# Kernel optimization log

Measured on AMD Instinct MI355X. Metric: run time of the kernel, lower is better.

The kernel has to match this reference:

```python
import jax, jax.numpy as jnp
import numpy as np

EMB = 2048
N_HEADS = 32
N_KV_HEADS = 8
HEAD_DIM = EMB // N_HEADS
NUM_Q_PER_KV = N_HEADS // N_KV_HEADS


def setup_inputs() -> dict:
    key = jax.random.key(0)
    ks = jax.random.split(key, 7)
    B, S = 2, 2048
    scale = 1.0 / np.sqrt(EMB)
    return {
        "query": jax.random.normal(ks[0], (B, S, EMB), jnp.float32),
        "key": jax.random.normal(ks[1], (B, S, EMB), jnp.float32),
        "value": jax.random.normal(ks[2], (B, S, EMB), jnp.float32),
        "Wq": jax.random.normal(ks[3], (EMB, EMB), jnp.float32) * scale,
        "Wk": jax.random.normal(ks[4], (EMB, N_KV_HEADS * HEAD_DIM), jnp.float32) * scale,
        "Wv": jax.random.normal(ks[5], (EMB, N_KV_HEADS * HEAD_DIM), jnp.float32) * scale,
        "Wo": jax.random.normal(ks[6], (EMB, EMB), jnp.float32) * scale,
    }


def reference(query, key, value, Wq, Wk, Wv, Wo):
    B, Sq, _ = query.shape
    Skv = key.shape[1]
    # projections (Linear, no bias)
    q = (query @ Wq).reshape(B, Sq, N_HEADS, HEAD_DIM)            # [B,Sq,H,D]
    k = (key @ Wk).reshape(B, Skv, N_KV_HEADS, HEAD_DIM)          # [B,Skv,Hkv,D]
    v = (value @ Wv).reshape(B, Skv, N_KV_HEADS, HEAD_DIM)
    # repeat_kv: expand each kv head to num_q_per_kv query heads
    k = jnp.repeat(k, NUM_Q_PER_KV, axis=2)                       # [B,Skv,H,D]
    v = jnp.repeat(v, NUM_Q_PER_KV, axis=2)
    # attention
    scores = jnp.einsum('bqhd,bkhd->bhqk', q, k) / np.sqrt(HEAD_DIM)
    probs = jax.nn.softmax(scores, axis=-1)                       # [B,H,Sq,Skv]
    ctx = jnp.einsum('bhqk,bkhd->bqhd', probs, v)                 # [B,Sq,H,D]
    ctx = ctx.reshape(B, Sq, EMB)
    return ctx @ Wo
```

## Files before the change

kernel.cpp:

```cpp
#include <hip/hip_runtime.h>
#include <hip/hip_bf16.h>
#include <stdint.h>

#define EMB   2048
#define HQ    32
#define NKV   8
#define HD    64
#define BATCH 2
#define SEQ   2048
#define MR    (BATCH * SEQ)
#define KVD   (NKV * HD)

using bfrag = __attribute__((ext_vector_type(8))) short;
using facc  = __attribute__((ext_vector_type(4))) float;

__device__ __forceinline__ unsigned short f32_bf16(float f) {
  union { float f; uint32_t u; } v;
  v.f = f;
  return (unsigned short)((v.u + 0x7fffu + ((v.u >> 16) & 1u)) >> 16);
}
__device__ __forceinline__ uint32_t pk2(float a, float b) {
  __hip_bfloat162 h = __float22bfloat162_rn(make_float2(a, b));
  uint32_t u; __builtin_memcpy(&u, &h, 4); return u;
}
__device__ __forceinline__ float fexp2(float x) {
#if __has_builtin(__builtin_amdgcn_exp2f)
  return __builtin_amdgcn_exp2f(x);
#else
  return exp2f(x);
#endif
}

__device__ __forceinline__ void gl2lds16(const void* g, void* l) {
  __builtin_amdgcn_global_load_lds((__attribute__((address_space(1))) void*)g,
                                   (__attribute__((address_space(3))) void*)l,
                                   16, 0, 0);
}

__device__ __forceinline__ void swz_mn_n(int bid, int nwg, int& m0, int& n0) {
  const int sw = (bid & 7) * (nwg >> 3) + (bid >> 3);
  m0 = (sw & 31) << 7;
  n0 = (sw >> 5) << 7;
}

__global__ __launch_bounds__(256) void kprep(const float* __restrict__ q_in,
                                             unsigned short* __restrict__ qbf,
                                             const float* __restrict__ Wq,
                                             const float* __restrict__ Wk,
                                             const float* __restrict__ Wv,
                                             const float* __restrict__ Wo,
                                             unsigned short* __restrict__ WqT,
                                             unsigned short* __restrict__ WkT,
                                             unsigned short* __restrict__ WvT,
                                             unsigned short* __restrict__ WoT,
                                             float qscale) {
  __shared__ unsigned short t[32][33];
  int bid = blockIdx.x;
  if (bid < 4096) {
    const size_t i0 = ((size_t)bid * 256 + threadIdx.x) * 8;
    const float4 f0 = *(const float4*)(q_in + i0);
    const float4 f1 = *(const float4*)(q_in + i0 + 4);
    uint4 w;
    w.x = pk2(f0.x * qscale, f0.y * qscale);
    w.y = pk2(f0.z * qscale, f0.w * qscale);
    w.z = pk2(f1.x * qscale, f1.y * qscale);
    w.w = pk2(f1.z * qscale, f1.w * qscale);
    *(uint4*)(qbf + i0) = w;
    return;
  }
  bid -= 4096;
  const float* in; unsigned short* out; int C;
  if (bid < 4096)      { in = Wq; out = WqT; C = 2048; }
  else if (bid < 5120) { bid -= 4096; in = Wk; out = WkT; C = 512; }
  else if (bid < 6144) { bid -= 5120; in = Wv; out = WvT; C = 512; }
  else                 { bid -= 6144; in = Wo; out = WoT; C = 2048; }
  const int R = 2048, CB = C >> 5;
  const int c0 = (bid % CB) * 32, r0 = (bid / CB) * 32;
  const int tx = threadIdx.x & 31, ty = threadIdx.x >> 5;
#pragma unroll
  for (int i = 0; i < 32; i += 8)
    t[ty + i][tx] = f32_bf16(in[(size_t)(r0 + ty + i) * C + (c0 + tx)]);
  __syncthreads();
#pragma unroll
  for (int i = 0; i < 32; i += 8)
    out[(size_t)(c0 + ty + i) * R + (r0 + tx)] = t[tx][ty + i];
}

__global__ __launch_bounds__(256) void kproj(const unsigned short* __restrict__ qbf,
                                             const float* __restrict__ k_in,
                                             const float* __restrict__ v_in,
                                             const unsigned short* __restrict__ WqT,
                                             const unsigned short* __restrict__ WkT,
                                             const unsigned short* __restrict__ WvT,
                                             unsigned short* __restrict__ qp,
                                             unsigned short* __restrict__ kp,
                                             unsigned short* __restrict__ vT) {
  __shared__ __align__(16) unsigned short As[128][32];
  __shared__ __align__(16) unsigned short Bs[128][32];
  int bid = blockIdx.x;
  int mode, N, lnwg;
  const unsigned short* Bt;
  if (bid < 512)      { mode = 0; Bt = WqT; N = 2048; lnwg = 512; }
  else if (bid < 640) { mode = 1; Bt = WkT; N = 512; lnwg = 128; bid -= 512; }
  else                { mode = 2; Bt = WvT; N = 512; lnwg = 128; bid -= 640; }
  int m0, n0; swz_mn_n(bid, lnwg, m0, n0);

  const int tid  = threadIdx.x;
  const int wv   = tid >> 6;
  const int lane = tid & 63;
  const int quad = lane >> 4;
  const int l15  = lane & 15;
  const int wm = (wv >> 1) * 64;
  const int wn = (wv & 1) * 64;
  const int K = EMB;

  const facc fzero = {0.f, 0.f, 0.f, 0.f};
  facc acc[4][4];
#pragma unroll
  for (int i = 0; i < 4; ++i)
#pragma unroll
    for (int j = 0; j < 4; ++j) acc[i][j] = fzero;

  const float* ain = (mode == 1) ? k_in : v_in;
  const int e0 = wv * 1024 + lane * 8;
  for (int k0 = 0; k0 < K; k0 += 32) {
    if (mode == 0) {
#pragma unroll
      for (int u = 0; u < 2; ++u) {
        const int e = e0 + u * 512;
        const int r = e >> 5, c = e & 31;
        gl2lds16(qbf + (size_t)(m0 + r) * K + (k0 + c), (unsigned short*)As + e);
        gl2lds16(Bt  + (size_t)(n0 + r) * K + (k0 + c), (unsigned short*)Bs + e);
      }
    } else {
#pragma unroll
      for (int u = 0; u < 2; ++u) {
        const int e = e0 + u * 512;
        const int r = e >> 5, c = e & 31;
        gl2lds16(Bt + (size_t)(n0 + r) * K + (k0 + c), (unsigned short*)Bs + e);
        const float* ap = ain + (size_t)(m0 + r) * K + (k0 + c);
        const float4 f0 = *(const float4*)ap;
        const float4 f1 = *(const float4*)(ap + 4);
        uint4 w;
        w.x = pk2(f0.x, f0.y);
        w.y = pk2(f0.z, f0.w);
        w.z = pk2(f1.x, f1.y);
        w.w = pk2(f1.z, f1.w);
        *(uint4*)((unsigned short*)As + e) = w;
      }
    }
    __syncthreads();
    bfrag af[4], bf[4];
#pragma unroll
    for (int i = 0; i < 4; ++i) af[i] = *(const bfrag*)&As[wm + i * 16 + l15][quad * 8];
#pragma unroll
    for (int j = 0; j < 4; ++j) bf[j] = *(const bfrag*)&Bs[wn + j * 16 + l15][quad * 8];
#pragma unroll
    for (int i = 0; i < 4; ++i)
#pragma unroll
      for (int j = 0; j < 4; ++j)
        acc[i][j] = __builtin_amdgcn_mfma_f32_16x16x32_bf16(af[i], bf[j], acc[i][j], 0, 0, 0);
    __syncthreads();
  }

  if (mode < 2) {
    unsigned short* Cp = (mode == 0) ? qp : kp;
#pragma unroll
    for (int i = 0; i < 4; ++i)
#pragma unroll
      for (int j = 0; j < 4; ++j) {
        const int col = n0 + wn + j * 16 + l15;
        const size_t base = (size_t)(m0 + wm + i * 16 + quad * 4) * N + col;
#pragma unroll
        for (int r = 0; r < 4; ++r)
          Cp[base + (size_t)r * N] = f32_bf16(acc[i][j][r]);
      }
  } else {
#pragma unroll
    for (int i = 0; i < 4; ++i)
#pragma unroll
      for (int j = 0; j < 4; ++j) {
        const int n = n0 + wn + j * 16 + l15;
        const int m = m0 + wm + i * 16 + quad * 4;
        uint2 w;
        w.x = pk2(acc[i][j][0], acc[i][j][1]);
        w.y = pk2(acc[i][j][2], acc[i][j][3]);
        *(uint2*)(vT + (size_t)n * MR + m) = w;
      }
  }
}

__global__ __launch_bounds__(256) void kgemm_bt_f32out(const unsigned short* __restrict__ A,
                                                       const unsigned short* __restrict__ Bt,
                                                       float* __restrict__ C,
                                                       int M, int N, int K) {
  __shared__ __align__(16) unsigned short As[128][32];
  __shared__ __align__(16) unsigned short Bs[128][32];
  const int tid  = threadIdx.x;
  const int wv   = tid >> 6;
  const int lane = tid & 63;
  const int quad = lane >> 4;
  const int l15  = lane & 15;
  int m0, n0; swz_mn_n(blockIdx.x, gridDim.x, m0, n0);
  const int wm = (wv >> 1) * 64;
  const int wn = (wv & 1) * 64;

  const facc fzero = {0.f, 0.f, 0.f, 0.f};
  facc acc[4][4];
#pragma unroll
  for (int i = 0; i < 4; ++i)
#pragma unroll
    for (int j = 0; j < 4; ++j) acc[i][j] = fzero;

  const int e0 = wv * 1024 + lane * 8;
  for (int k0 = 0; k0 < K; k0 += 32) {
#pragma unroll
    for (int u = 0; u < 2; ++u) {
      const int e = e0 + u * 512;
      const int r = e >> 5, c = e & 31;
      gl2lds16(A  + (size_t)(m0 + r) * K + (k0 + c), (unsigned short*)As + e);
      gl2lds16(Bt + (size_t)(n0 + r) * K + (k0 + c), (unsigned short*)Bs + e);
    }
    __syncthreads();
    bfrag af[4], bf[4];
#pragma unroll
    for (int i = 0; i < 4; ++i) af[i] = *(const bfrag*)&As[wm + i * 16 + l15][quad * 8];
#pragma unroll
    for (int j = 0; j < 4; ++j) bf[j] = *(const bfrag*)&Bs[wn + j * 16 + l15][quad * 8];
#pragma unroll
    for (int i = 0; i < 4; ++i)
#pragma unroll
      for (int j = 0; j < 4; ++j)
        acc[i][j] = __builtin_amdgcn_mfma_f32_16x16x32_bf16(af[i], bf[j], acc[i][j], 0, 0, 0);
    __syncthreads();
  }

#pragma unroll
  for (int i = 0; i < 4; ++i)
#pragma unroll
    for (int j = 0; j < 4; ++j) {
      const int col = n0 + wn + j * 16 + l15;
      const size_t base = (size_t)(m0 + wm + i * 16 + quad * 4) * N + col;
#pragma unroll
      for (int r = 0; r < 4; ++r)
        C[base + (size_t)r * N] = acc[i][j][r];
    }
}

__device__ __forceinline__ unsigned short* psa(unsigned short* p, int row, int colShort) {
  return (unsigned short*)((char*)p + ((row << 7) + (((colShort << 1)) ^ ((row & 7) << 4))));
}
__device__ __forceinline__ const bfrag* tfrag(const unsigned short* base, int r, int c) {
  return (const bfrag*)(base + (size_t)r * 64 + ((c ^ (r & 7)) << 3));
}

__global__ __launch_bounds__(128, 2) void kattn(const unsigned short* __restrict__ Qp,
                                                const unsigned short* __restrict__ Kp,
                                                const unsigned short* __restrict__ Vt,
                                                unsigned short* __restrict__ Ctx) {
  __shared__ __align__(16) unsigned short Ps[2][64][64];
  __shared__ __align__(16) unsigned short Kb[2][64 * 64];
  __shared__ __align__(16) unsigned short Vs[64 * 64];

  const int tid  = threadIdx.x;
  const int wv   = tid >> 6;
  const int lane = tid & 63;
  const int quad = lane >> 4;
  const int l15  = lane & 15;
  const int q0  = blockIdx.x * 128;
  const int h   = blockIdx.y;
  const int b   = blockIdx.z;
  const int kvh = h >> 2;

  unsigned short* ps = &Ps[wv][0][0];

  const unsigned short* qbase = Qp + (size_t)(b * SEQ + q0 + wv * 64) * EMB + h * HD;
  bfrag qf[2][4];
#pragma unroll
  for (int kk = 0; kk < 2; ++kk)
#pragma unroll
    for (int j = 0; j < 4; ++j)
      qf[kk][j] = *(const bfrag*)(qbase + (size_t)(j * 16 + l15) * EMB + kk * 32 + quad * 8);

  const facc fzero = {0.f, 0.f, 0.f, 0.f};
  float l_st[4];
  facc o[4][4];
#pragma unroll
  for (int j = 0; j < 4; ++j) l_st[j] = 0.f;
#pragma unroll
  for (int i = 0; i < 4; ++i)
#pragma unroll
    for (int j = 0; j < 4; ++j) o[i][j] = fzero;

  const unsigned short* kg = Kp + (size_t)(b * SEQ) * KVD + kvh * HD;
  const unsigned short* vg = Vt + (size_t)(kvh * HD) * MR + b * SEQ;
  const int r8  = lane >> 3;
  const int sc8 = ((lane & 7) ^ r8) * 8;

#pragma unroll
  for (int u = 0; u < 4; ++u) {
    const int row = (wv * 4 + u) * 8 + r8;
    gl2lds16(kg + (size_t)row * KVD + sc8, &Kb[0][(wv * 4 + u) * 512]);
  }

  for (int kt = 0; kt < SEQ / 64; ++kt) {
    const int cur = kt & 1;
    __asm__ __volatile__("s_waitcnt vmcnt(0)" ::: "memory");
    __builtin_amdgcn_s_barrier();
    __asm__ __volatile__("" ::: "memory");

#pragma unroll
    for (int u = 0; u < 4; ++u) {
      const int row = (wv * 4 + u) * 8 + r8;
      gl2lds16(vg + (size_t)row * MR + kt * 64 + sc8, &Vs[(wv * 4 + u) * 512]);
    }
    const int ktn = (kt < SEQ / 64 - 1) ? kt + 1 : kt;
#pragma unroll
    for (int u = 0; u < 4; ++u) {
      const int row = (wv * 4 + u) * 8 + r8;
      gl2lds16(kg + (size_t)(ktn * 64 + row) * KVD + sc8, &Kb[cur ^ 1][(wv * 4 + u) * 512]);
    }

    const unsigned short* kb = &Kb[cur][0];
    float rs[4] = {0.f, 0.f, 0.f, 0.f};
#pragma unroll
    for (int i = 0; i < 4; ++i) {
      const bfrag af0 = *tfrag(kb, i * 16 + l15, quad);
      const bfrag af1 = *tfrag(kb, i * 16 + l15, 4 + quad);
      facc s[4];
#pragma unroll
      for (int j = 0; j < 4; ++j) s[j] = fzero;
      __builtin_amdgcn_s_setprio(1);
#pragma unroll
      for (int j = 0; j < 4; ++j)
        s[j] = __builtin_amdgcn_mfma_f32_16x16x32_bf16(af0, qf[0][j], s[j], 0, 0, 0);
#pragma unroll
      for (int j = 0; j < 4; ++j)
        s[j] = __builtin_amdgcn_mfma_f32_16x16x32_bf16(af1, qf[1][j], s[j], 0, 0, 0);
      __builtin_amdgcn_s_setprio(0);
#pragma unroll
      for (int j = 0; j < 4; ++j) {
        const float p0 = fexp2(s[j][0]);
        const float p1 = fexp2(s[j][1]);
        const float p2 = fexp2(s[j][2]);
        const float p3 = fexp2(s[j][3]);
        rs[j] += (p0 + p1) + (p2 + p3);
        uint2 w;
        w.x = pk2(p0, p1);
        w.y = pk2(p2, p3);
        *(uint2*)psa(ps, j * 16 + l15, i * 16 + quad * 4) = w;
      }
    }

#pragma unroll
    for (int j = 0; j < 4; ++j) {
      float r = rs[j];
      r += __shfl_xor(r, 16, 64);
      r += __shfl_xor(r, 32, 64);
      l_st[j] += r;
    }

    __asm__ __volatile__("s_waitcnt vmcnt(4)" ::: "memory");
    __builtin_amdgcn_s_barrier();
    __asm__ __volatile__("" ::: "memory");

    __builtin_amdgcn_s_setprio(1);
#pragma unroll
    for (int kk = 0; kk < 2; ++kk) {
      bfrag bpf[4], vf[4];
#pragma unroll
      for (int j = 0; j < 4; ++j)
        bpf[j] = *(const bfrag*)psa(ps, j * 16 + l15, kk * 32 + quad * 8);
#pragma unroll
      for (int id = 0; id < 4; ++id)
        vf[id] = *tfrag(Vs, id * 16 + l15, kk * 4 + quad);
#pragma unroll
      for (int id = 0; id < 4; ++id)
#pragma unroll
        for (int j = 0; j < 4; ++j)
          o[id][j] = __builtin_amdgcn_mfma_f32_16x16x32_bf16(vf[id], bpf[j], o[id][j], 0, 0, 0);
    }
    __builtin_amdgcn_s_setprio(0);
  }

#pragma unroll
  for (int j = 0; j < 4; ++j) {
    const float inv = 1.f / l_st[j];
#pragma unroll
    for (int id = 0; id < 4; ++id) {
      uint2 w;
      w.x = pk2(o[id][j][0] * inv, o[id][j][1] * inv);
      w.y = pk2(o[id][j][2] * inv, o[id][j][3] * inv);
      *(uint2*)psa(ps, j * 16 + l15, id * 16 + quad * 4) = w;
    }
  }
  __asm__ __volatile__("" ::: "memory");
#pragma unroll
  for (int s = 0; s < 8; ++s) {
    const int r  = (lane >> 2) + 16 * (s & 3);
    const int cb = (lane & 3) * 8 + 32 * (s >> 2);
    const uint4 t = *(const uint4*)psa(ps, r, cb);
    const size_t row = (size_t)(b * SEQ + q0 + wv * 64 + r);
    *(uint4*)&Ctx[row * EMB + h * HD + cb] = t;
  }
}

extern "C" void kernel_launch(void* const* d_in, const int* in_sizes, int n_in,
                              void* d_out, int out_size, void* d_ws, size_t ws_size,
                              hipStream_t stream) {
  (void)in_sizes; (void)n_in; (void)out_size; (void)ws_size;
  const float* q_in = (const float*)d_in[0];
  const float* k_in = (const float*)d_in[1];
  const float* v_in = (const float*)d_in[2];
  const float* Wq   = (const float*)d_in[3];
  const float* Wk   = (const float*)d_in[4];
  const float* Wv   = (const float*)d_in[5];
  const float* Wo   = (const float*)d_in[6];
  float* out = (float*)d_out;

  char* ws = (char*)d_ws;
  unsigned short* WqT = (unsigned short*)(ws);
  unsigned short* WkT = (unsigned short*)(ws + (size_t)( 8u << 20));
  unsigned short* WvT = (unsigned short*)(ws + (size_t)(10u << 20));
  unsigned short* WoT = (unsigned short*)(ws + (size_t)(12u << 20));
  unsigned short* qbf = (unsigned short*)(ws + (size_t)(20u << 20));
  unsigned short* qp  = (unsigned short*)(ws + (size_t)(36u << 20));
  unsigned short* kp  = (unsigned short*)(ws + (size_t)(52u << 20));
  unsigned short* vT  = (unsigned short*)(ws + (size_t)(56u << 20));
  unsigned short* ctx = qbf;

  kprep<<<14336, 256, 0, stream>>>(q_in, qbf, Wq, Wk, Wv, Wo,
                                   WqT, WkT, WvT, WoT, 0.18033688011112042f);
  kproj<<<768, 256, 0, stream>>>(qbf, k_in, v_in, WqT, WkT, WvT, qp, kp, vT);
  kattn<<<dim3(16, 32, 2), 128, 0, stream>>>(qp, kp, vT, ctx);
  kgemm_bt_f32out<<<512, 256, 0, stream>>>(ctx, WoT, out, MR, EMB, EMB);
}
```

Measured before the change: 396.5 us.

## Double-buffer LDS tiles in Q projection and output GEMM loops

Adds a second LDS buffer for the A and B tiles in the Q-projection path of kproj and in the output-projection GEMM. The next K-slice is prefetched with direct global-to-LDS loads while MFMAs consume the current slice, and one barrier per iteration is removed. The goal is to hide global load latency behind compute. LDS use per block doubles, which may reduce occupancy. Correctness depends on the async gl2lds load completing before the single barrier at the end of each iteration.

```diff
diff --git a/kernel.cpp b/kernel.cpp
--- a/kernel.cpp
+++ b/kernel.cpp
@@ -95,8 +95,8 @@
                                              unsigned short* __restrict__ qp,
                                              unsigned short* __restrict__ kp,
                                              unsigned short* __restrict__ vT) {
-  __shared__ __align__(16) unsigned short As[128][32];
-  __shared__ __align__(16) unsigned short Bs[128][32];
+  __shared__ __align__(16) unsigned short As[2][4096];
+  __shared__ __align__(16) unsigned short Bs[2][4096];
   int bid = blockIdx.x;
   int mode, N, lnwg;
   const unsigned short* Bt;
@@ -121,23 +121,53 @@
 #pragma unroll
     for (int j = 0; j < 4; ++j) acc[i][j] = fzero;
 
-  const float* ain = (mode == 1) ? k_in : v_in;
   const int e0 = wv * 1024 + lane * 8;
-  for (int k0 = 0; k0 < K; k0 += 32) {
-    if (mode == 0) {
+
+  if (mode == 0) {
+#pragma unroll
+    for (int u = 0; u < 2; ++u) {
+      const int e = e0 + u * 512;
+      const int r = e >> 5, c = e & 31;
+      gl2lds16(qbf + (size_t)(m0 + r) * K + c, &As[0][e]);
+      gl2lds16(Bt  + (size_t)(n0 + r) * K + c, &Bs[0][e]);
+    }
+    __syncthreads();
+    int cur = 0;
+    const int NT = K >> 5;
+    for (int t = 0; t < NT; ++t) {
+      if (t + 1 < NT) {
+        const int k1 = (t + 1) << 5;
+#pragma unroll
+        for (int u = 0; u < 2; ++u) {
+          const int e = e0 + u * 512;
+          const int r = e >> 5, c = e & 31;
+          gl2lds16(qbf + (size_t)(m0 + r) * K + k1 + c, &As[cur ^ 1][e]);
+          gl2lds16(Bt  + (size_t)(n0 + r) * K + k1 + c, &Bs[cur ^ 1][e]);
+        }
+      }
+      bfrag af[4], bf[4];
+#pragma unroll
+      for (int i = 0; i < 4; ++i)
+        af[i] = *(const bfrag*)&As[cur][(wm + i * 16 + l15) * 32 + quad * 8];
+#pragma unroll
+      for (int j = 0; j < 4; ++j)
+        bf[j] = *(const bfrag*)&Bs[cur][(wn + j * 16 + l15) * 32 + quad * 8];
+#pragma unroll
+      for (int i = 0; i < 4; ++i)
+#pragma unroll
+        for (int j = 0; j < 4; ++j)
+          acc[i][j] = __builtin_amdgcn_mfma_f32_16x16x32_bf16(af[i], bf[j], acc[i][j], 0, 0, 0);
+      __syncthreads();
+      cur ^= 1;
+    }
+  } else {
+    const float* ain = (mode == 1) ? k_in : v_in;
+    for (int k0 = 0; k0 < K; k0 += 32) {
 #pragma unroll
       for (int u = 0; u < 2; ++u) {
         const int e = e0 + u * 512;
         const int r = e >> 5, c = e & 31;
-        gl2lds16(qbf + (size_t)(m0 + r) * K + (k0 + c), (unsigned short*)As + e);
-        gl2lds16(Bt  + (size_t)(n0 + r) * K + (k0 + c), (unsigned short*)Bs + e);
-      }
-    } else {
-#pragma unroll
-      for (int u = 0; u < 2; ++u) {
-        const int e = e0 + u * 512;
-        const int r = e >> 5, c = e & 31;
-        gl2lds16(Bt + (size_t)(n0 + r) * K + (k0 + c), (unsigned short*)Bs + e);
+        gl2lds16(Bt + (size_t)(n0 + r) * K + (k0 + c), &Bs[0][e]);
         const float* ap = ain + (size_t)(m0 + r) * K + (k0 + c);
         const float4 f0 = *(const float4*)ap;
         const float4 f1 = *(const float4*)(ap + 4);
@@ -146,21 +176,23 @@
         w.y = pk2(f0.z, f0.w);
         w.z = pk2(f1.x, f1.y);
         w.w = pk2(f1.z, f1.w);
-        *(uint4*)((unsigned short*)As + e) = w;
-      }
-    }
-    __syncthreads();
-    bfrag af[4], bf[4];
-#pragma unroll
-    for (int i = 0; i < 4; ++i) af[i] = *(const bfrag*)&As[wm + i * 16 + l15][quad * 8];
-#pragma unroll
-    for (int j = 0; j < 4; ++j) bf[j] = *(const bfrag*)&Bs[wn + j * 16 + l15][quad * 8];
-#pragma unroll
-    for (int i = 0; i < 4; ++i)
-#pragma unroll
-      for (int j = 0; j < 4; ++j)
-        acc[i][j] = __builtin_amdgcn_mfma_f32_16x16x32_bf16(af[i], bf[j], acc[i][j], 0, 0, 0);
-    __syncthreads();
+        *(uint4*)&As[0][e] = w;
+      }
+      __syncthreads();
+      bfrag af[4], bf[4];
+#pragma unroll
+      for (int i = 0; i < 4; ++i)
+        af[i] = *(const bfrag*)&As[0][(wm + i * 16 + l15) * 32 + quad * 8];
+#pragma unroll
+      for (int j = 0; j < 4; ++j)
+        bf[j] = *(const bfrag*)&Bs[0][(wn + j * 16 + l15) * 32 + quad * 8];
+#pragma unroll
+      for (int i = 0; i < 4; ++i)
+#pragma unroll
+        for (int j = 0; j < 4; ++j)
+          acc[i][j] = __builtin_amdgcn_mfma_f32_16x16x32_bf16(af[i], bf[j], acc[i][j], 0, 0, 0);
+      __syncthreads();
+    }
   }
 
   if (mode < 2) {
@@ -194,8 +226,8 @@
                                                        const unsigned short* __restrict__ Bt,
                                                        float* __restrict__ C,
                                                        int M, int N, int K) {
-  __shared__ __align__(16) unsigned short As[128][32];
-  __shared__ __align__(16) unsigned short Bs[128][32];
+  __shared__ __align__(16) unsigned short As[2][4096];
+  __shared__ __align__(16) unsigned short Bs[2][4096];
   const int tid  = threadIdx.x;
   const int wv   = tid >> 6;
   const int lane = tid & 63;
@@ -213,26 +245,41 @@
     for (int j = 0; j < 4; ++j) acc[i][j] = fzero;
 
   const int e0 = wv * 1024 + lane * 8;
-  for (int k0 = 0; k0 < K; k0 += 32) {
-#pragma unroll
-    for (int u = 0; u < 2; ++u) {
-      const int e = e0 + u * 512;
-      const int r = e >> 5, c = e & 31;
-      gl2lds16(A  + (size_t)(m0 + r) * K + (k0 + c), (unsigned short*)As + e);
-      gl2lds16(Bt + (size_t)(n0 + r) * K + (k0 + c), (unsigned short*)Bs + e);
-    }
-    __syncthreads();
+#pragma unroll
+  for (int u = 0; u < 2; ++u) {
+    const int e = e0 + u * 512;
+    const int r = e >> 5, c = e & 31;
+    gl2lds16(A  + (size_t)(m0 + r) * K + c, &As[0][e]);
+    gl2lds16(Bt + (size_t)(n0 + r) * K + c, &Bs[0][e]);
+  }
+  __syncthreads();
+  int cur = 0;
+  const int NT = K >> 5;
+  for (int t = 0; t < NT; ++t) {
+    if (t + 1 < NT) {
+      const int k1 = (t + 1) << 5;
+#pragma unroll
+      for (int u = 0; u < 2; ++u) {
+        const int e = e0 + u * 512;
+        const int r = e >> 5, c = e & 31;
+        gl2lds16(A  + (size_t)(m0 + r) * K + k1 + c, &As[cur ^ 1][e]);
+        gl2lds16(Bt + (size_t)(n0 + r) * K + k1 + c, &Bs[cur ^ 1][e]);
+      }
+    }
     bfrag af[4], bf[4];
 #pragma unroll
-    for (int i = 0; i < 4; ++i) af[i] = *(const bfrag*)&As[wm + i * 16 + l15][quad * 8];
-#pragma unroll
-    for (int j = 0; j < 4; ++j) bf[j] = *(const bfrag*)&Bs[wn + j * 16 + l15][quad * 8];
+    for (int i = 0; i < 4; ++i)
+      af[i] = *(const bfrag*)&As[cur][(wm + i * 16 + l15) * 32 + quad * 8];
+#pragma unroll
+    for (int j = 0; j < 4; ++j)
+      bf[j] = *(const bfrag*)&Bs[cur][(wn + j * 16 + l15) * 32 + quad * 8];
 #pragma unroll
     for (int i = 0; i < 4; ++i)
 #pragma unroll
       for (int j = 0; j < 4; ++j)
         acc[i][j] = __builtin_amdgcn_mfma_f32_16x16x32_bf16(af[i], bf[j], acc[i][j], 0, 0, 0);
     __syncthreads();
+    cur ^= 1;
   }
 
 #pragma unroll
```

New measurement: 397.9 us. About the same (+0.3%).

## Double GEMM K-tile to 64 with XOR-swizzled LDS layout in projection kernels

Applied to the files above, without the earlier changes.

Both projection GEMM kernels now stage a 64-wide K slice per iteration instead of 32, which halves the number of barrier pairs per tile and gives each wave twice as many MFMAs between barriers. The LDS tiles are stored with an XOR swizzle on 16-byte chunks, and the global column read is permuted to match, so fragment reads are meant to avoid bank conflicts. The cost is double the LDS use per block (32 KB), which may lower occupancy, plus more live fragment registers.

```diff
diff --git a/kernel.cpp b/kernel.cpp
--- a/kernel.cpp
+++ b/kernel.cpp
@@ -41,6 +41,10 @@
   const int sw = (bid & 7) * (nwg >> 3) + (bid >> 3);
   m0 = (sw & 31) << 7;
   n0 = (sw >> 5) << 7;
+}
+
+__device__ __forceinline__ const bfrag* tfrag(const unsigned short* base, int r, int c) {
+  return (const bfrag*)(base + (size_t)r * 64 + ((c ^ (r & 7)) << 3));
 }
 
 __global__ __launch_bounds__(256) void kprep(const float* __restrict__ q_in,
@@ -95,8 +99,8 @@
                                              unsigned short* __restrict__ qp,
                                              unsigned short* __restrict__ kp,
                                              unsigned short* __restrict__ vT) {
-  __shared__ __align__(16) unsigned short As[128][32];
-  __shared__ __align__(16) unsigned short Bs[128][32];
+  __shared__ __align__(16) unsigned short As[128 * 64];
+  __shared__ __align__(16) unsigned short Bs[128 * 64];
   int bid = blockIdx.x;
   int mode, N, lnwg;
   const unsigned short* Bt;
@@ -114,6 +118,9 @@
   const int wn = (wv & 1) * 64;
   const int K = EMB;
 
+  const int strow = tid >> 3;
+  const int swc   = (((tid & 7) ^ (strow & 7)) << 3);
+
   const facc fzero = {0.f, 0.f, 0.f, 0.f};
   facc acc[4][4];
 #pragma unroll
@@ -122,23 +129,22 @@
     for (int j = 0; j < 4; ++j) acc[i][j] = fzero;
 
   const float* ain = (mode == 1) ? k_in : v_in;
-  const int e0 = wv * 1024 + lane * 8;
-  for (int k0 = 0; k0 < K; k0 += 32) {
+  for (int k0 = 0; k0 < K; k0 += 64) {
     if (mode == 0) {
 #pragma unroll
-      for (int u = 0; u < 2; ++u) {
-        const int e = e0 + u * 512;
-        const int r = e >> 5, c = e & 31;
-        gl2lds16(qbf + (size_t)(m0 + r) * K + (k0 + c), (unsigned short*)As + e);
-        gl2lds16(Bt  + (size_t)(n0 + r) * K + (k0 + c), (unsigned short*)Bs + e);
+      for (int u = 0; u < 4; ++u) {
+        const int r   = u * 32 + strow;
+        const int eld = u * 2048 + tid * 8;
+        gl2lds16(qbf + (size_t)(m0 + r) * K + k0 + swc, As + eld);
+        gl2lds16(Bt  + (size_t)(n0 + r) * K + k0 + swc, Bs + eld);
       }
     } else {
 #pragma unroll
-      for (int u = 0; u < 2; ++u) {
-        const int e = e0 + u * 512;
-        const int r = e >> 5, c = e & 31;
-        gl2lds16(Bt + (size_t)(n0 + r) * K + (k0 + c), (unsigned short*)Bs + e);
-        const float* ap = ain + (size_t)(m0 + r) * K + (k0 + c);
+      for (int u = 0; u < 4; ++u) {
+        const int r   = u * 32 + strow;
+        const int eld = u * 2048 + tid * 8;
+        gl2lds16(Bt + (size_t)(n0 + r) * K + k0 + swc, Bs + eld);
+        const float* ap = ain + (size_t)(m0 + r) * K + k0 + swc;
         const float4 f0 = *(const float4*)ap;
         const float4 f1 = *(const float4*)(ap + 4);
         uint4 w;
@@ -146,20 +152,25 @@
         w.y = pk2(f0.z, f0.w);
         w.z = pk2(f1.x, f1.y);
         w.w = pk2(f1.z, f1.w);
-        *(uint4*)((unsigned short*)As + e) = w;
+        *(uint4*)(As + eld) = w;
       }
     }
     __syncthreads();
-    bfrag af[4], bf[4];
-#pragma unroll
-    for (int i = 0; i < 4; ++i) af[i] = *(const bfrag*)&As[wm + i * 16 + l15][quad * 8];
-#pragma unroll
-    for (int j = 0; j < 4; ++j) bf[j] = *(const bfrag*)&Bs[wn + j * 16 + l15][quad * 8];
-#pragma unroll
-    for (int i = 0; i < 4; ++i)
-#pragma unroll
-      for (int j = 0; j < 4; ++j)
-        acc[i][j] = __builtin_amdgcn_mfma_f32_16x16x32_bf16(af[i], bf[j], acc[i][j], 0, 0, 0);
+    bfrag af[2][4], bf[2][4];
+#pragma unroll
+    for (int kk = 0; kk < 2; ++kk)
+#pragma unroll
+      for (int i = 0; i < 4; ++i) {
+        af[kk][i] = *tfrag(As, wm + i * 16 + l15, kk * 4 + quad);
+        bf[kk][i] = *tfrag(Bs, wn + i * 16 + l15, kk * 4 + quad);
+      }
+#pragma unroll
+    for (int kk = 0; kk < 2; ++kk)
+#pragma unroll
+      for (int i = 0; i < 4; ++i)
+#pragma unroll
+        for (int j = 0; j < 4; ++j)
+          acc[i][j] = __builtin_amdgcn_mfma_f32_16x16x32_bf16(af[kk][i], bf[kk][j], acc[i][j], 0, 0, 0);
     __syncthreads();
   }
 
@@ -194,8 +205,8 @@
                                                        const unsigned short* __restrict__ Bt,
                                                        float* __restrict__ C,
                                                        int M, int N, int K) {
-  __shared__ __align__(16) unsigned short As[128][32];
-  __shared__ __align__(16) unsigned short Bs[128][32];
+  __shared__ __align__(16) unsigned short As[128 * 64];
+  __shared__ __align__(16) unsigned short Bs[128 * 64];
   const int tid  = threadIdx.x;
   const int wv   = tid >> 6;
   const int lane = tid & 63;
@@ -205,6 +216,9 @@
   const int wm = (wv >> 1) * 64;
   const int wn = (wv & 1) * 64;
 
+  const int strow = tid >> 3;
+  const int swc   = (((tid & 7) ^ (strow & 7)) << 3);
+
   const facc fzero = {0.f, 0.f, 0.f, 0.f};
   facc acc[4][4];
 #pragma unroll
@@ -212,26 +226,30 @@
 #pragma unroll
     for (int j = 0; j < 4; ++j) acc[i][j] = fzero;
 
-  const int e0 = wv * 1024 + lane * 8;
-  for (int k0 = 0; k0 < K; k0 += 32) {
-#pragma unroll
-    for (int u = 0; u < 2; ++u) {
-      const int e = e0 + u * 512;
-      const int r = e >> 5, c = e & 31;
-      gl2lds16(A  + (size_t)(m0 + r) * K + (k0 + c), (unsigned short*)As + e);
-      gl2lds16(Bt + (size_t)(n0 + r) * K + (k0 + c), (unsigned short*)Bs + e);
+  for (int k0 = 0; k0 < K; k0 += 64) {
+#pragma unroll
+    for (int u = 0; u < 4; ++u) {
+      const int r   = u * 32 + strow;
+      const int eld = u * 2048 + tid * 8;
+      gl2lds16(A  + (size_t)(m0 + r) * K + k0 + swc, As + eld);
+      gl2lds16(Bt + (size_t)(n0 + r) * K + k0 + swc, Bs + eld);
     }
     __syncthreads();
-    bfrag af[4], bf[4];
-#pragma unroll
-    for (int i = 0; i < 4; ++i) af[i] = *(const bfrag*)&As[wm + i * 16 + l15][quad * 8];
-#pragma unroll
-    for (int j = 0; j < 4; ++j) bf[j] = *(const bfrag*)&Bs[wn + j * 16 + l15][quad * 8];
-#pragma unroll
-    for (int i = 0; i < 4; ++i)
-#pragma unroll
-      for (int j = 0; j < 4; ++j)
-        acc[i][j] = __builtin_amdgcn_mfma_f32_16x16x32_bf16(af[i], bf[j], acc[i][j], 0, 0, 0);
+    bfrag af[2][4], bf[2][4];
+#pragma unroll
+    for (int kk = 0; kk < 2; ++kk)
+#pragma unroll
+      for (int i = 0; i < 4; ++i) {
+        af[kk][i] = *tfrag(As, wm + i * 16 + l15, kk * 4 + quad);
+        bf[kk][i] = *tfrag(Bs, wn + i * 16 + l15, kk * 4 + quad);
+      }
+#pragma unroll
+    for (int kk = 0; kk < 2; ++kk)
+#pragma unroll
+      for (int i = 0; i < 4; ++i)
+#pragma unroll
+        for (int j = 0; j < 4; ++j)
+          acc[i][j] = __builtin_amdgcn_mfma_f32_16x16x32_bf16(af[kk][i], bf[kk][j], acc[i][j], 0, 0, 0);
     __syncthreads();
   }
 
@@ -249,9 +267,6 @@
 
 __device__ __forceinline__ unsigned short* psa(unsigned short* p, int row, int colShort) {
   return (unsigned short*)((char*)p + ((row << 7) + (((colShort << 1)) ^ ((row & 7) << 4))));
-}
-__device__ __forceinline__ const bfrag* tfrag(const unsigned short* base, int r, int c) {
-  return (const bfrag*)(base + (size_t)r * 64 + ((c ^ (r & 7)) << 3));
 }
 
 __global__ __launch_bounds__(128, 2) void kattn(const unsigned short* __restrict__ Qp,
```

New measurement: 371.4 us. 1.07x faster.
